# Optimization experiments

Hardware: AMD Instinct MI355X
Metric: run time of the kernel (lower is better)

The kernel has to match this reference:

```python
import jax, jax.numpy as jnp
import numpy as np

N, E, DIN, DH, DOUT, G = 100000, 1600000, 128, 128, 40, 512


def setup_inputs() -> dict:
    key = jax.random.key(0)
    ks = jax.random.split(key, 8)
    x = jax.random.normal(ks[0], (N, DIN), dtype=jnp.float32)
    src = jax.random.randint(ks[1], (E,), 0, N)
    dst = jax.random.randint(ks[2], (E,), 0, N)
    batch = jnp.sort(jax.random.randint(ks[3], (N,), 0, G))
    W1 = jax.random.normal(ks[4], (DIN, DH), dtype=jnp.float32) * (1.0 / np.sqrt(DIN))
    b1 = jnp.zeros((DH,), dtype=jnp.float32)
    W2 = jax.random.normal(ks[5], (DH, DOUT), dtype=jnp.float32) * (1.0 / np.sqrt(DH))
    b2 = jnp.zeros((DOUT,), dtype=jnp.float32)
    return {"x": x, "src": src, "dst": dst, "batch": batch,
            "W1": W1, "b1": b1, "W2": W2, "b2": b2, "num_graphs": G}


def gcn_conv(h, src, dst, n, W, b):
    # PyG GCNConv: linear transform, then D^-1/2 (A + I) D^-1/2 aggregation.
    h = h @ W  # [n, d_out]
    # degree on destination nodes, including self-loop weight 1
    deg = jax.ops.segment_sum(jnp.ones_like(dst, dtype=h.dtype), dst, num_segments=n) + 1.0
    dinv = jax.lax.rsqrt(deg)  # deg >= 1 so always finite
    coef = dinv[src] * dinv[dst]  # [E]
    agg = jax.ops.segment_sum(h[src] * coef[:, None], dst, num_segments=n)
    agg = agg + h * (dinv * dinv)[:, None]  # self-loop term
    return agg + b


def reference(x, src, dst, batch, W1, b1, W2, b2, num_graphs):
    n = x.shape[0]
    h = jax.nn.relu(gcn_conv(x, src, dst, n, W1, b1))  # dropout = identity (eval mode)
    h = jax.nn.relu(gcn_conv(h, src, dst, n, W2, b2))
    # global mean pool over graphs in the batch
    cnt = jax.ops.segment_sum(jnp.ones((n,), dtype=h.dtype), batch, num_segments=num_graphs)
    pooled = jax.ops.segment_sum(h, batch, num_segments=num_graphs) / jnp.maximum(cnt, 1.0)[:, None]
    return jax.nn.log_softmax(pooled, axis=1)
```

## Files before the change

### kernel.cpp

```cpp
#include <hip/hip_runtime.h>
#include <math.h>


typedef __attribute__((ext_vector_type(4))) float f32x4;
typedef __attribute__((ext_vector_type(2))) float f32x2;
typedef __attribute__((ext_vector_type(8))) short bf16x8;
typedef __attribute__((ext_vector_type(4))) uint uint4v;
typedef __attribute__((ext_vector_type(2))) uint uint2v;

constexpr int PAD = 64;
constexpr int CAP = 1536;
constexpr int NBMAX = 1600;

static __device__ __forceinline__ ushort f2bf(float f) {
    union { float f; uint u; } v{f};
    uint r = (v.u + 0x7FFF + ((v.u >> 16) & 1)) >> 16;
    return (ushort)r;
}
static __device__ __forceinline__ float bflo(uint v) {
    union { uint u; float f; } o{v << 16};
    return o.f;
}
static __device__ __forceinline__ float bfhi(uint v) {
    union { uint u; float f; } o{v & 0xffff0000u};
    return o.f;
}
static __device__ __forceinline__ uint packbf(float lo, float hi) {
    return ((uint)f2bf(hi) << 16) | (uint)f2bf(lo);
}

__global__ __launch_bounds__(1024) void k_binhist(
    const int* __restrict__ src, const int* __restrict__ dst, int E, int nbkt,
    int* __restrict__ cur2, int* __restrict__ bins,
    const float* __restrict__ W1, const float* __restrict__ W2,
    ushort* __restrict__ w1t, ushort* __restrict__ w2t, int histB) {
    __shared__ int lc[NBMAX];
    const int bid = blockIdx.x;
    const int t = threadIdx.x;
    if (bid >= histB) {
        int i = (bid - histB) * 1024 + t;
        if (i < 128 * 128) {
            int n = i >> 7, k = i & 127;
            w1t[i] = f2bf(W1[k * 128 + n]);
        } else if (i < 128 * 128 + 64 * 128) {
            int j = i - 128 * 128;
            int n = j >> 7, k = j & 127;
            w2t[j] = (n < 40) ? f2bf(W2[k * 40 + n]) : (ushort)0;
        }
        return;
    }
    for (int b = t; b < nbkt; b += 1024) lc[b] = 0;
    __syncthreads();
    const int elo = (int)(((long long)E * bid) / histB);
    const int ehi = (int)(((long long)E * (bid + 1)) / histB);
    for (int e = elo + t; e < ehi; e += 1024) {
        int d = __builtin_nontemporal_load(&dst[e]);
        atomicAdd(&lc[d >> 6], 1);
    }
    __syncthreads();
    for (int b = t; b < nbkt; b += 1024) {
        int c = lc[b];
        lc[b] = (c > 0) ? atomicAdd(&cur2[b], c) : 0;
    }
    __syncthreads();
    for (int e = elo + t; e < ehi; e += 1024) {
        int d = __builtin_nontemporal_load(&dst[e]);
        int s = __builtin_nontemporal_load(&src[e]);
        int b = d >> 6;
        int pos = atomicAdd(&lc[b], 1);
        if (pos < CAP) bins[(size_t)b * CAP + pos] = ((d & 63) << 17) | s;
    }
}

__global__ __launch_bounds__(256) void k_fillb(const int* __restrict__ cur2,
                                               const int* __restrict__ bins,
                                               int* __restrict__ degi,
                                               int* __restrict__ colidx, int N) {
    __shared__ int lcnt[64];
    const int b = blockIdx.x;
    const int base = b << 6;
    const int t = threadIdx.x;
    if (t < 64) lcnt[t] = 0;
    __syncthreads();
    int cnt = min(cur2[b], CAP);
    for (int i = t; i < cnt; i += 256) {
        int entry = bins[(size_t)b * CAP + i];
        int d = entry >> 17;
        int s = entry & 0x1FFFF;
        int r = atomicAdd(&lcnt[d], 1);
        if (r < PAD) colidx[((base + d) << 6) + r] = s;
    }
    __syncthreads();
    if (t < 64 && base + t < N) degi[base + t] = lcnt[t];
}

__global__ __launch_bounds__(256) void k_gemm1(const float* __restrict__ A,
                                               const ushort* __restrict__ BT,
                                               const int* __restrict__ degi,
                                               uint* __restrict__ g1u, int M) {
    __shared__ ushort As[64][136];
    __shared__ ushort Bs[128][136];
    const int tid = threadIdx.x;
    const int m0 = blockIdx.x * 64;
#pragma unroll
    for (int i = 0; i < 4; i++) {
        int chunk = tid + i * 256;
        int r = chunk >> 4, c8 = chunk & 15;
        float4 v0 = {0.f, 0.f, 0.f, 0.f}, v1 = {0.f, 0.f, 0.f, 0.f};
        if (m0 + r < M) {
            const float* p = &A[(size_t)(m0 + r) * 128 + c8 * 8];
            v0 = *(const float4*)p;
            v1 = *(const float4*)(p + 4);
        }
        ushort o[8];
        o[0] = f2bf(v0.x); o[1] = f2bf(v0.y); o[2] = f2bf(v0.z); o[3] = f2bf(v0.w);
        o[4] = f2bf(v1.x); o[5] = f2bf(v1.y); o[6] = f2bf(v1.z); o[7] = f2bf(v1.w);
        *(float4*)&As[r][c8 * 8] = *(float4*)o;
    }
#pragma unroll
    for (int i = 0; i < 8; i++) {
        int chunk = tid + i * 256;
        int r = chunk >> 4, c = chunk & 15;
        *(float4*)&Bs[r][c * 8] = *(const float4*)&BT[(size_t)r * 128 + c * 8];
    }
    __syncthreads();
    const int wave = tid >> 6, lane = tid & 63;
    const int arow = wave * 16 + (lane & 15);
    const int kgrp = (lane >> 4) * 8;
    f32x4 acc[8];
#pragma unroll
    for (int i = 0; i < 8; i++) acc[i] = (f32x4){0.f, 0.f, 0.f, 0.f};
#pragma unroll
    for (int kk = 0; kk < 4; kk++) {
        bf16x8 a = *(const bf16x8*)&As[arow][kk * 32 + kgrp];
#pragma unroll
        for (int nf = 0; nf < 8; nf++) {
            bf16x8 b = *(const bf16x8*)&Bs[nf * 16 + (lane & 15)][kk * 32 + kgrp];
            acc[nf] = __builtin_amdgcn_mfma_f32_16x16x32_bf16(b, a, acc[nf], 0, 0, 0);
        }
    }
    const int m = m0 + wave * 16 + (lane & 15);
    float dv = (m < M) ? rsqrtf((float)degi[m] + 1.0f) : 0.f;
#pragma unroll
    for (int nf = 0; nf < 8; nf++) {
        uint u = __builtin_amdgcn_cvt_pk_fp8_f32(dv * acc[nf][0], dv * acc[nf][1],
                                                 0, false);
        u = (uint)__builtin_amdgcn_cvt_pk_fp8_f32(dv * acc[nf][2], dv * acc[nf][3],
                                                  (int)u, true);
        if (m < M) g1u[(size_t)m * 32 + nf * 4 + (lane >> 4)] = u;
    }
}

__global__ __launch_bounds__(256) void k_agg128(const uint* __restrict__ g1u,
                                                const int* __restrict__ degi,
                                                const int* __restrict__ colidx,
                                                const float* __restrict__ bias,
                                                ushort* __restrict__ hout, int N) {
    __shared__ int sidx[4][64];
    const int w = threadIdx.x >> 6;
    const int lane = threadIdx.x & 63;
    const int wid = (blockIdx.x * 256 + threadIdx.x) >> 6;
    if (wid >= N) return;
    const int q = lane >> 4;
    const int l16 = lane & 15;
    const uint2v* hu = (const uint2v*)g1u;
    const int dg = degi[wid];
    const int cnt = min(dg, PAD);
    const int beg = wid << 6;
    float a0 = 0.f, a1 = 0.f, a2 = 0.f, a3 = 0.f;
    float a4 = 0.f, a5 = 0.f, a6 = 0.f, a7 = 0.f;
    if (lane < cnt) sidx[w][lane] = colidx[beg + lane];
    int i = 0;
    for (; i + 16 <= cnt; i += 16) {
        uint2v v[4];
#pragma unroll
        for (int k = 0; k < 4; k++) {
            v[k] = hu[(size_t)sidx[w][i + 4 * k + q] * 16 + l16];
        }
#pragma unroll
        for (int k = 0; k < 4; k++) {
            f32x2 d0 = __builtin_amdgcn_cvt_pk_f32_fp8(v[k].x, false);
            f32x2 d1 = __builtin_amdgcn_cvt_pk_f32_fp8(v[k].x, true);
            f32x2 d2 = __builtin_amdgcn_cvt_pk_f32_fp8(v[k].y, false);
            f32x2 d3 = __builtin_amdgcn_cvt_pk_f32_fp8(v[k].y, true);
            a0 += d0.x; a1 += d0.y; a2 += d1.x; a3 += d1.y;
            a4 += d2.x; a5 += d2.y; a6 += d3.x; a7 += d3.y;
        }
    }
    for (; i + q < cnt; i += 4) {
        uint2v vv = hu[(size_t)sidx[w][i + q] * 16 + l16];
        f32x2 d0 = __builtin_amdgcn_cvt_pk_f32_fp8(vv.x, false);
        f32x2 d1 = __builtin_amdgcn_cvt_pk_f32_fp8(vv.x, true);
        f32x2 d2 = __builtin_amdgcn_cvt_pk_f32_fp8(vv.y, false);
        f32x2 d3 = __builtin_amdgcn_cvt_pk_f32_fp8(vv.y, true);
        a0 += d0.x; a1 += d0.y; a2 += d1.x; a3 += d1.y;
        a4 += d2.x; a5 += d2.y; a6 += d3.x; a7 += d3.y;
    }
    a0 += __shfl_xor(a0, 16); a1 += __shfl_xor(a1, 16);
    a2 += __shfl_xor(a2, 16); a3 += __shfl_xor(a3, 16);
    a4 += __shfl_xor(a4, 16); a5 += __shfl_xor(a5, 16);
    a6 += __shfl_xor(a6, 16); a7 += __shfl_xor(a7, 16);
    a0 += __shfl_xor(a0, 32); a1 += __shfl_xor(a1, 32);
    a2 += __shfl_xor(a2, 32); a3 += __shfl_xor(a3, 32);
    a4 += __shfl_xor(a4, 32); a5 += __shfl_xor(a5, 32);
    a6 += __shfl_xor(a6, 32); a7 += __shfl_xor(a7, 32);
    if (lane < 16) {
        float dn = rsqrtf((float)dg + 1.0f);
        uint2v sv = hu[(size_t)wid * 16 + l16];
        {
            f32x2 d0 = __builtin_amdgcn_cvt_pk_f32_fp8(sv.x, false);
            f32x2 d1 = __builtin_amdgcn_cvt_pk_f32_fp8(sv.x, true);
            f32x2 d2 = __builtin_amdgcn_cvt_pk_f32_fp8(sv.y, false);
            f32x2 d3 = __builtin_amdgcn_cvt_pk_f32_fp8(sv.y, true);
            a0 += d0.x; a1 += d0.y; a2 += d1.x; a3 += d1.y;
            a4 += d2.x; a5 += d2.y; a6 += d3.x; a7 += d3.y;
        }
        float4 b0 = *(const float4*)&bias[l16 * 8];
        float4 b1v = *(const float4*)&bias[l16 * 8 + 4];
        a0 = dn * fmaxf(dn * a0 + b0.x, 0.f);
        a1 = dn * fmaxf(dn * a1 + b0.y, 0.f);
        a2 = dn * fmaxf(dn * a2 + b0.z, 0.f);
        a3 = dn * fmaxf(dn * a3 + b0.w, 0.f);
        a4 = dn * fmaxf(dn * a4 + b1v.x, 0.f);
        a5 = dn * fmaxf(dn * a5 + b1v.y, 0.f);
        a6 = dn * fmaxf(dn * a6 + b1v.z, 0.f);
        a7 = dn * fmaxf(dn * a7 + b1v.w, 0.f);
        uint4v o;
        o.x = packbf(a0, a1);
        o.y = packbf(a2, a3);
        o.z = packbf(a4, a5);
        o.w = packbf(a6, a7);
        __builtin_nontemporal_store(o, &((uint4v*)hout)[(size_t)wid * 16 + l16]);
    }
}

__global__ __launch_bounds__(256) void k_gemm_p(const ushort* __restrict__ A,
                                                const ushort* __restrict__ BT,
                                                uint* __restrict__ pu, int M) {
    __shared__ ushort As[64][136];
    __shared__ ushort Bs[64][136];
    const int tid = threadIdx.x;
    const int m0 = blockIdx.x * 64;
#pragma unroll
    for (int i = 0; i < 4; i++) {
        int chunk = tid + i * 256;
        int r = chunk >> 4, c = chunk & 15;
        float4 v = {0.f, 0.f, 0.f, 0.f};
        if (m0 + r < M) v = *(const float4*)&A[((size_t)(m0 + r)) * 128 + c * 8];
        *(float4*)&As[r][c * 8] = v;
    }
#pragma unroll
    for (int i = 0; i < 4; i++) {
        int chunk = tid + i * 256;
        int r = chunk >> 4, c = chunk & 15;
        *(float4*)&Bs[r][c * 8] = *(const float4*)&BT[(size_t)r * 128 + c * 8];
    }
    __syncthreads();
    const int wave = tid >> 6, lane = tid & 63;
    const int arow = wave * 16 + (lane & 15);
    const int kgrp = (lane >> 4) * 8;
    f32x4 acc[4];
#pragma unroll
    for (int i = 0; i < 4; i++) acc[i] = (f32x4){0.f, 0.f, 0.f, 0.f};
#pragma unroll
    for (int kk = 0; kk < 4; kk++) {
        bf16x8 a = *(const bf16x8*)&As[arow][kk * 32 + kgrp];
#pragma unroll
        for (int nf = 0; nf < 4; nf++) {
            bf16x8 b = *(const bf16x8*)&Bs[nf * 16 + (lane & 15)][kk * 32 + kgrp];
            acc[nf] = __builtin_amdgcn_mfma_f32_16x16x32_bf16(b, a, acc[nf], 0, 0, 0);
        }
    }
    const int m = m0 + wave * 16 + (lane & 15);
#pragma unroll
    for (int nf = 0; nf < 4; nf++) {
        uint u = __builtin_amdgcn_cvt_pk_fp8_f32(acc[nf][0], acc[nf][1], 0, false);
        u = (uint)__builtin_amdgcn_cvt_pk_fp8_f32(acc[nf][2], acc[nf][3], (int)u, true);
        if (m < M) pu[(size_t)m * 16 + nf * 4 + (lane >> 4)] = u;
    }
}

__global__ __launch_bounds__(256) void k_agg40(const uint* __restrict__ pu,
                                               const int* __restrict__ degi,
                                               const int* __restrict__ colidx,
                                               const float* __restrict__ b2,
                                               float* __restrict__ h2a, int N) {
    __shared__ int sidx[4][64];
    const int w = threadIdx.x >> 6;
    const int lane = threadIdx.x & 63;
    const int wid = (blockIdx.x * 256 + threadIdx.x) >> 6;
    if (wid >= N) return;
    const int q = lane >> 4;
    const int l16 = lane & 15;
    const int dg = degi[wid];
    const int cnt = min(dg, PAD);
    const int beg = wid << 6;
    float a0 = 0.f, a1 = 0.f, a2 = 0.f, a3 = 0.f;
    if (lane < cnt) sidx[w][lane] = colidx[beg + lane];
    int i = 0;
    for (; i + 16 <= cnt; i += 16) {
        uint v[4];
#pragma unroll
        for (int k = 0; k < 4; k++) {
            v[k] = pu[(size_t)sidx[w][i + 4 * k + q] * 16 + l16];
        }
#pragma unroll
        for (int k = 0; k < 4; k++) {
            f32x2 d0 = __builtin_amdgcn_cvt_pk_f32_fp8(v[k], false);
            f32x2 d1 = __builtin_amdgcn_cvt_pk_f32_fp8(v[k], true);
            a0 += d0.x; a1 += d0.y; a2 += d1.x; a3 += d1.y;
        }
    }
    for (; i + q < cnt; i += 4) {
        uint vv = pu[(size_t)sidx[w][i + q] * 16 + l16];
        f32x2 d0 = __builtin_amdgcn_cvt_pk_f32_fp8(vv, false);
        f32x2 d1 = __builtin_amdgcn_cvt_pk_f32_fp8(vv, true);
        a0 += d0.x; a1 += d0.y; a2 += d1.x; a3 += d1.y;
    }
    a0 += __shfl_xor(a0, 16); a1 += __shfl_xor(a1, 16);
    a2 += __shfl_xor(a2, 16); a3 += __shfl_xor(a3, 16);
    a0 += __shfl_xor(a0, 32); a1 += __shfl_xor(a1, 32);
    a2 += __shfl_xor(a2, 32); a3 += __shfl_xor(a3, 32);
    if (lane < 16 && l16 < 10) {
        float dn = rsqrtf((float)dg + 1.0f);
        uint sv = pu[(size_t)wid * 16 + l16];
        f32x2 d0 = __builtin_amdgcn_cvt_pk_f32_fp8(sv, false);
        f32x2 d1 = __builtin_amdgcn_cvt_pk_f32_fp8(sv, true);
        a0 += d0.x; a1 += d0.y; a2 += d1.x; a3 += d1.y;
        float4 bb = *(const float4*)&b2[l16 * 4];
        float4 o;
        o.x = fmaxf(dn * a0 + bb.x, 0.f);
        o.y = fmaxf(dn * a1 + bb.y, 0.f);
        o.z = fmaxf(dn * a2 + bb.z, 0.f);
        o.w = fmaxf(dn * a3 + bb.w, 0.f);
        *(float4*)&h2a[(size_t)wid * 40 + l16 * 4] = o;
    }
}

__global__ __launch_bounds__(256) void k_pool(const float* __restrict__ h2a,
                                              const int* __restrict__ batch, int N,
                                              int DOUT, float* __restrict__ out) {
    int g = blockIdx.x;
    int t = threadIdx.x;
    int lo = 0, hi = N;
    while (lo < hi) {
        int mid = (lo + hi) >> 1;
        if (batch[mid] < g) lo = mid + 1; else hi = mid;
    }
    int start = lo;
    hi = N;
    while (lo < hi) {
        int mid = (lo + hi) >> 1;
        if (batch[mid] <= g) lo = mid + 1; else hi = mid;
    }
    int end = lo;
    int cnt = end - start;
    int c = t & 63, rr = t >> 6;
    float acc = 0.f;
    if (c < DOUT) {
        for (int i = start + rr; i < end; i += 4) acc += h2a[(size_t)i * DOUT + c];
    }
    __shared__ float sm[4][64];
    sm[rr][c] = acc;
    __syncthreads();
    if (t < 64) {
        float v = (c < DOUT)
                      ? (sm[0][c] + sm[1][c] + sm[2][c] + sm[3][c]) / fmaxf((float)cnt, 1.f)
                      : -1e30f;
        float m = v;
#pragma unroll
        for (int o = 32; o; o >>= 1) m = fmaxf(m, __shfl_xor(m, o));
        float ex = (c < DOUT) ? expf(v - m) : 0.f;
        float s = ex;
#pragma unroll
        for (int o = 32; o; o >>= 1) s += __shfl_xor(s, o);
        if (c < DOUT) out[g * DOUT + c] = (v - m) - logf(s);
    }
}

extern "C" void kernel_launch(void* const* d_in, const int* in_sizes, int n_in,
                              void* d_out, int out_size, void* d_ws, size_t ws_size,
                              hipStream_t stream) {
    const float* x = (const float*)d_in[0];
    const int* src = (const int*)d_in[1];
    const int* dst = (const int*)d_in[2];
    const int* batch = (const int*)d_in[3];
    const float* W1 = (const float*)d_in[4];
    const float* b1 = (const float*)d_in[5];
    const float* W2 = (const float*)d_in[6];
    const float* b2 = (const float*)d_in[7];
    float* out = (float*)d_out;

    const int N = in_sizes[3];
    const int E = in_sizes[1];
    const int DOUT = in_sizes[7];
    const int G = out_size / DOUT;
    const int nbkt = (N + 63) >> 6;

    char* ws = (char*)d_ws;
    size_t off = 0;
    auto alloc = [&](size_t bytes) -> char* {
        char* p = ws + off;
        off += (bytes + 255) & ~(size_t)255;
        return p;
    };
    uint* g1u = (uint*)alloc((size_t)N * 128);
    ushort* g2 = (ushort*)alloc((size_t)N * 128 * 2);
    int* colidx = (int*)alloc((size_t)N * PAD * 4);
    int* bins = (int*)alloc((size_t)nbkt * CAP * 4);
    ushort* w1t = (ushort*)alloc(128 * 128 * 2);
    ushort* w2t = (ushort*)alloc(64 * 128 * 2);
    int* degi = (int*)alloc((size_t)N * 4);
    float* h2a = (float*)alloc((size_t)N * 40 * 4);
    char* z0 = ws + off;
    int* cur2 = (int*)alloc((size_t)nbkt * 4);
    size_t zlen = (size_t)((ws + off) - z0);

    uint* pu = g1u;

    hipMemsetAsync(z0, 0, zlen, stream);

    const int TB = 256;
    const int histB = 256;
    const int prepB = (128 * 128 + 64 * 128 + 1023) / 1024;
    k_binhist<<<histB + prepB, 1024, 0, stream>>>(src, dst, E, nbkt, cur2, bins,
                                                  W1, W2, w1t, w2t, histB);
    k_fillb<<<nbkt, TB, 0, stream>>>(cur2, bins, degi, colidx, N);
    k_gemm1<<<(N + 63) / 64, TB, 0, stream>>>(x, w1t, degi, g1u, N);
    k_agg128<<<(N + 3) / 4, TB, 0, stream>>>(g1u, degi, colidx, b1, g2, N);
    k_gemm_p<<<(N + 63) / 64, TB, 0, stream>>>(g2, w2t, pu, N);
    k_agg40<<<(N + 3) / 4, TB, 0, stream>>>(pu, degi, colidx, b2, h2a, N);
    k_pool<<<G, TB, 0, stream>>>(h2a, batch, N, DOUT, out);
}
```

Baseline: 191.7 us.

## Fuse layer-1 aggregation with layer-2 GEMM into a single kernel

Merges the 128-wide neighbor aggregation kernel with the following bf16 MFMA projection. Each block aggregates 16 nodes into a shared-memory tile and multiplies it by W2 there, so the bf16 intermediate no longer makes a round trip through global memory and one launch disappears. The fp8 accumulation is also rewritten to add packed float2 vectors directly, which may let the compiler emit packed adds. In exchange, each block does 16 rows, each wave walks four nodes in sequence, and every block reloads W2 into LDS, which raises LDS use and may reduce occupancy and latency hiding for the gathers.

Measured after the change: 189.7 us. Within noise of the previous version (-1.0%).

```diff
diff --git a/kernel.cpp b/kernel.cpp
--- a/kernel.cpp
+++ b/kernel.cpp
@@ -16,14 +16,6 @@
     union { float f; uint u; } v{f};
     uint r = (v.u + 0x7FFF + ((v.u >> 16) & 1)) >> 16;
     return (ushort)r;
-}
-static __device__ __forceinline__ float bflo(uint v) {
-    union { uint u; float f; } o{v << 16};
-    return o.f;
-}
-static __device__ __forceinline__ float bfhi(uint v) {
-    union { uint u; float f; } o{v & 0xffff0000u};
-    return o.f;
 }
 static __device__ __forceinline__ uint packbf(float lo, float hi) {
     return ((uint)f2bf(hi) << 16) | (uint)f2bf(lo);
@@ -151,133 +143,111 @@
     }
 }
 
-__global__ __launch_bounds__(256) void k_agg128(const uint* __restrict__ g1u,
-                                                const int* __restrict__ degi,
-                                                const int* __restrict__ colidx,
-                                                const float* __restrict__ bias,
-                                                ushort* __restrict__ hout, int N) {
+__global__ __launch_bounds__(256) void k_agg1p(const uint* __restrict__ g1u,
+                                               const int* __restrict__ degi,
+                                               const int* __restrict__ colidx,
+                                               const float* __restrict__ bias,
+                                               const ushort* __restrict__ w2t,
+                                               uint* __restrict__ pu, int N) {
+    __shared__ ushort g2t[16][136];
+    __shared__ ushort Bs[64][136];
     __shared__ int sidx[4][64];
-    const int w = threadIdx.x >> 6;
-    const int lane = threadIdx.x & 63;
-    const int wid = (blockIdx.x * 256 + threadIdx.x) >> 6;
-    if (wid >= N) return;
+    const int tid = threadIdx.x;
+    const int w = tid >> 6;
+    const int lane = tid & 63;
     const int q = lane >> 4;
     const int l16 = lane & 15;
     const uint2v* hu = (const uint2v*)g1u;
-    const int dg = degi[wid];
-    const int cnt = min(dg, PAD);
-    const int beg = wid << 6;
-    float a0 = 0.f, a1 = 0.f, a2 = 0.f, a3 = 0.f;
-    float a4 = 0.f, a5 = 0.f, a6 = 0.f, a7 = 0.f;
-    if (lane < cnt) sidx[w][lane] = colidx[beg + lane];
-    int i = 0;
-    for (; i + 16 <= cnt; i += 16) {
-        uint2v v[4];
-#pragma unroll
-        for (int k = 0; k < 4; k++) {
-            v[k] = hu[(size_t)sidx[w][i + 4 * k + q] * 16 + l16];
-        }
-#pragma unroll
-        for (int k = 0; k < 4; k++) {
-            f32x2 d0 = __builtin_amdgcn_cvt_pk_f32_fp8(v[k].x, false);
-            f32x2 d1 = __builtin_amdgcn_cvt_pk_f32_fp8(v[k].x, true);
-            f32x2 d2 = __builtin_amdgcn_cvt_pk_f32_fp8(v[k].y, false);
-            f32x2 d3 = __builtin_amdgcn_cvt_pk_f32_fp8(v[k].y, true);
-            a0 += d0.x; a1 += d0.y; a2 += d1.x; a3 += d1.y;
-            a4 += d2.x; a5 += d2.y; a6 += d3.x; a7 += d3.y;
-        }
-    }
-    for (; i + q < cnt; i += 4) {
-        uint2v vv = hu[(size_t)sidx[w][i + q] * 16 + l16];
-        f32x2 d0 = __builtin_amdgcn_cvt_pk_f32_fp8(vv.x, false);
-        f32x2 d1 = __builtin_amdgcn_cvt_pk_f32_fp8(vv.x, true);
-        f32x2 d2 = __builtin_amdgcn_cvt_pk_f32_fp8(vv.y, false);
-        f32x2 d3 = __builtin_amdgcn_cvt_pk_f32_fp8(vv.y, true);
-        a0 += d0.x; a1 += d0.y; a2 += d1.x; a3 += d1.y;
-        a4 += d2.x; a5 += d2.y; a6 += d3.x; a7 += d3.y;
-    }
-    a0 += __shfl_xor(a0, 16); a1 += __shfl_xor(a1, 16);
-    a2 += __shfl_xor(a2, 16); a3 += __shfl_xor(a3, 16);
-    a4 += __shfl_xor(a4, 16); a5 += __shfl_xor(a5, 16);
-    a6 += __shfl_xor(a6, 16); a7 += __shfl_xor(a7, 16);
-    a0 += __shfl_xor(a0, 32); a1 += __shfl_xor(a1, 32);
-    a2 += __shfl_xor(a2, 32); a3 += __shfl_xor(a3, 32);
-    a4 += __shfl_xor(a4, 32); a5 += __shfl_xor(a5, 32);
-    a6 += __shfl_xor(a6, 32); a7 += __shfl_xor(a7, 32);
-    if (lane < 16) {
-        float dn = rsqrtf((float)dg + 1.0f);
-        uint2v sv = hu[(size_t)wid * 16 + l16];
-        {
-            f32x2 d0 = __builtin_amdgcn_cvt_pk_f32_fp8(sv.x, false);
-            f32x2 d1 = __builtin_amdgcn_cvt_pk_f32_fp8(sv.x, true);
-            f32x2 d2 = __builtin_amdgcn_cvt_pk_f32_fp8(sv.y, false);
-            f32x2 d3 = __builtin_amdgcn_cvt_pk_f32_fp8(sv.y, true);
-            a0 += d0.x; a1 += d0.y; a2 += d1.x; a3 += d1.y;
-            a4 += d2.x; a5 += d2.y; a6 += d3.x; a7 += d3.y;
-        }
-        float4 b0 = *(const float4*)&bias[l16 * 8];
-        float4 b1v = *(const float4*)&bias[l16 * 8 + 4];
-        a0 = dn * fmaxf(dn * a0 + b0.x, 0.f);
-        a1 = dn * fmaxf(dn * a1 + b0.y, 0.f);
-        a2 = dn * fmaxf(dn * a2 + b0.z, 0.f);
-        a3 = dn * fmaxf(dn * a3 + b0.w, 0.f);
-        a4 = dn * fmaxf(dn * a4 + b1v.x, 0.f);
-        a5 = dn * fmaxf(dn * a5 + b1v.y, 0.f);
-        a6 = dn * fmaxf(dn * a6 + b1v.z, 0.f);
-        a7 = dn * fmaxf(dn * a7 + b1v.w, 0.f);
-        uint4v o;
-        o.x = packbf(a0, a1);
-        o.y = packbf(a2, a3);
-        o.z = packbf(a4, a5);
-        o.w = packbf(a6, a7);
-        __builtin_nontemporal_store(o, &((uint4v*)hout)[(size_t)wid * 16 + l16]);
-    }
-}
-
-__global__ __launch_bounds__(256) void k_gemm_p(const ushort* __restrict__ A,
-                                                const ushort* __restrict__ BT,
-                                                uint* __restrict__ pu, int M) {
-    __shared__ ushort As[64][136];
-    __shared__ ushort Bs[64][136];
-    const int tid = threadIdx.x;
-    const int m0 = blockIdx.x * 64;
+    const int tile0 = blockIdx.x * 16;
 #pragma unroll
     for (int i = 0; i < 4; i++) {
         int chunk = tid + i * 256;
         int r = chunk >> 4, c = chunk & 15;
-        float4 v = {0.f, 0.f, 0.f, 0.f};
-        if (m0 + r < M) v = *(const float4*)&A[((size_t)(m0 + r)) * 128 + c * 8];
-        *(float4*)&As[r][c * 8] = v;
-    }
-#pragma unroll
-    for (int i = 0; i < 4; i++) {
-        int chunk = tid + i * 256;
-        int r = chunk >> 4, c = chunk & 15;
-        *(float4*)&Bs[r][c * 8] = *(const float4*)&BT[(size_t)r * 128 + c * 8];
-    }
-    __syncthreads();
-    const int wave = tid >> 6, lane = tid & 63;
-    const int arow = wave * 16 + (lane & 15);
+        *(float4*)&Bs[r][c * 8] = *(const float4*)&w2t[(size_t)r * 128 + c * 8];
+    }
+#pragma unroll
+    for (int sub = 0; sub < 4; sub++) {
+        const int r = w * 4 + sub;
+        const int wid = tile0 + r;
+        f32x2 a0 = {0.f, 0.f}, a1 = {0.f, 0.f}, a2 = {0.f, 0.f}, a3 = {0.f, 0.f};
+        int dg = 0;
+        if (wid < N) {
+            dg = degi[wid];
+            const int cnt = min(dg, PAD);
+            const int beg = wid << 6;
+            if (lane < cnt) sidx[w][lane] = colidx[beg + lane];
+            int i = 0;
+            for (; i + 16 <= cnt; i += 16) {
+                uint2v v[4];
+#pragma unroll
+                for (int k = 0; k < 4; k++) {
+                    v[k] = hu[(size_t)sidx[w][i + 4 * k + q] * 16 + l16];
+                }
+#pragma unroll
+                for (int k = 0; k < 4; k++) {
+                    a0 += __builtin_amdgcn_cvt_pk_f32_fp8(v[k].x, false);
+                    a1 += __builtin_amdgcn_cvt_pk_f32_fp8(v[k].x, true);
+                    a2 += __builtin_amdgcn_cvt_pk_f32_fp8(v[k].y, false);
+                    a3 += __builtin_amdgcn_cvt_pk_f32_fp8(v[k].y, true);
+                }
+            }
+            for (; i + q < cnt; i += 4) {
+                uint2v vv = hu[(size_t)sidx[w][i + q] * 16 + l16];
+                a0 += __builtin_amdgcn_cvt_pk_f32_fp8(vv.x, false);
+                a1 += __builtin_amdgcn_cvt_pk_f32_fp8(vv.x, true);
+                a2 += __builtin_amdgcn_cvt_pk_f32_fp8(vv.y, false);
+                a3 += __builtin_amdgcn_cvt_pk_f32_fp8(vv.y, true);
+            }
+        }
+        a0.x += __shfl_xor(a0.x, 16); a0.y += __shfl_xor(a0.y, 16);
+        a1.x += __shfl_xor(a1.x, 16); a1.y += __shfl_xor(a1.y, 16);
+        a2.x += __shfl_xor(a2.x, 16); a2.y += __shfl_xor(a2.y, 16);
+        a3.x += __shfl_xor(a3.x, 16); a3.y += __shfl_xor(a3.y, 16);
+        a0.x += __shfl_xor(a0.x, 32); a0.y += __shfl_xor(a0.y, 32);
+        a1.x += __shfl_xor(a1.x, 32); a1.y += __shfl_xor(a1.y, 32);
+        a2.x += __shfl_xor(a2.x, 32); a2.y += __shfl_xor(a2.y, 32);
+        a3.x += __shfl_xor(a3.x, 32); a3.y += __shfl_xor(a3.y, 32);
+        if (lane < 16) {
+            float dn = rsqrtf((float)dg + 1.0f);
+            if (wid < N) {
+                uint2v sv = hu[(size_t)wid * 16 + l16];
+                a0 += __builtin_amdgcn_cvt_pk_f32_fp8(sv.x, false);
+                a1 += __builtin_amdgcn_cvt_pk_f32_fp8(sv.x, true);
+                a2 += __builtin_amdgcn_cvt_pk_f32_fp8(sv.y, false);
+                a3 += __builtin_amdgcn_cvt_pk_f32_fp8(sv.y, true);
+            }
+            float4 b0 = *(const float4*)&bias[l16 * 8];
+            float4 b1v = *(const float4*)&bias[l16 * 8 + 4];
+            float r0 = dn * fmaxf(dn * a0.x + b0.x, 0.f);
+            float r1 = dn * fmaxf(dn * a0.y + b0.y, 0.f);
+            float r2 = dn * fmaxf(dn * a1.x + b0.z, 0.f);
+            float r3 = dn * fmaxf(dn * a1.y + b0.w, 0.f);
+            float r4 = dn * fmaxf(dn * a2.x + b1v.x, 0.f);
+            float r5 = dn * fmaxf(dn * a2.y + b1v.y, 0.f);
+            float r6 = dn * fmaxf(dn * a3.x + b1v.z, 0.f);
+            float r7 = dn * fmaxf(dn * a3.y + b1v.w, 0.f);
+            uint4v o;
+            o.x = packbf(r0, r1);
+            o.y = packbf(r2, r3);
+            o.z = packbf(r4, r5);
+            o.w = packbf(r6, r7);
+            *(uint4v*)&g2t[r][l16 * 8] = o;
+        }
+    }
+    __syncthreads();
+    const int arow = lane & 15;
     const int kgrp = (lane >> 4) * 8;
-    f32x4 acc[4];
-#pragma unroll
-    for (int i = 0; i < 4; i++) acc[i] = (f32x4){0.f, 0.f, 0.f, 0.f};
+    f32x4 acc = {0.f, 0.f, 0.f, 0.f};
 #pragma unroll
     for (int kk = 0; kk < 4; kk++) {
-        bf16x8 a = *(const bf16x8*)&As[arow][kk * 32 + kgrp];
-#pragma unroll
-        for (int nf = 0; nf < 4; nf++) {
-            bf16x8 b = *(const bf16x8*)&Bs[nf * 16 + (lane & 15)][kk * 32 + kgrp];
-            acc[nf] = __builtin_amdgcn_mfma_f32_16x16x32_bf16(b, a, acc[nf], 0, 0, 0);
-        }
-    }
-    const int m = m0 + wave * 16 + (lane & 15);
-#pragma unroll
-    for (int nf = 0; nf < 4; nf++) {
-        uint u = __builtin_amdgcn_cvt_pk_fp8_f32(acc[nf][0], acc[nf][1], 0, false);
-        u = (uint)__builtin_amdgcn_cvt_pk_fp8_f32(acc[nf][2], acc[nf][3], (int)u, true);
-        if (m < M) pu[(size_t)m * 16 + nf * 4 + (lane >> 4)] = u;
-    }
+        bf16x8 a = *(const bf16x8*)&g2t[arow][kk * 32 + kgrp];
+        bf16x8 b = *(const bf16x8*)&Bs[w * 16 + (lane & 15)][kk * 32 + kgrp];
+        acc = __builtin_amdgcn_mfma_f32_16x16x32_bf16(b, a, acc, 0, 0, 0);
+    }
+    const int m = tile0 + (lane & 15);
+    uint u = __builtin_amdgcn_cvt_pk_fp8_f32(acc[0], acc[1], 0, false);
+    u = (uint)__builtin_amdgcn_cvt_pk_fp8_f32(acc[2], acc[3], (int)u, true);
+    if (m < N) pu[(size_t)m * 16 + w * 4 + (lane >> 4)] = u;
 }
 
 __global__ __launch_bounds__(256) void k_agg40(const uint* __restrict__ pu,
@@ -295,7 +265,7 @@
     const int dg = degi[wid];
     const int cnt = min(dg, PAD);
     const int beg = wid << 6;
-    float a0 = 0.f, a1 = 0.f, a2 = 0.f, a3 = 0.f;
+    f32x2 a01 = {0.f, 0.f}, a23 = {0.f, 0.f};
     if (lane < cnt) sidx[w][lane] = colidx[beg + lane];
     int i = 0;
     for (; i + 16 <= cnt; i += 16) {
@@ -306,33 +276,30 @@
         }
 #pragma unroll
         for (int k = 0; k < 4; k++) {
-            f32x2 d0 = __builtin_amdgcn_cvt_pk_f32_fp8(v[k], false);
-            f32x2 d1 = __builtin_amdgcn_cvt_pk_f32_fp8(v[k], true);
-            a0 += d0.x; a1 += d0.y; a2 += d1.x; a3 += d1.y;
+            a01 += __builtin_amdgcn_cvt_pk_f32_fp8(v[k], false);
+            a23 += __builtin_amdgcn_cvt_pk_f32_fp8(v[k], true);
         }
     }
     for (; i + q < cnt; i += 4) {
         uint vv = pu[(size_t)sidx[w][i + q] * 16 + l16];
-        f32x2 d0 = __builtin_amdgcn_cvt_pk_f32_fp8(vv, false);
-        f32x2 d1 = __builtin_amdgcn_cvt_pk_f32_fp8(vv, true);
-        a0 += d0.x; a1 += d0.y; a2 += d1.x; a3 += d1.y;
-    }
-    a0 += __shfl_xor(a0, 16); a1 += __shfl_xor(a1, 16);
-    a2 += __shfl_xor(a2, 16); a3 += __shfl_xor(a3, 16);
-    a0 += __shfl_xor(a0, 32); a1 += __shfl_xor(a1, 32);
-    a2 += __shfl_xor(a2, 32); a3 += __shfl_xor(a3, 32);
+        a01 += __builtin_amdgcn_cvt_pk_f32_fp8(vv, false);
+        a23 += __builtin_amdgcn_cvt_pk_f32_fp8(vv, true);
+    }
+    a01.x += __shfl_xor(a01.x, 16); a01.y += __shfl_xor(a01.y, 16);
+    a23.x += __shfl_xor(a23.x, 16); a23.y += __shfl_xor(a23.y, 16);
+    a01.x += __shfl_xor(a01.x, 32); a01.y += __shfl_xor(a01.y, 32);
+    a23.x += __shfl_xor(a23.x, 32); a23.y += __shfl_xor(a23.y, 32);
     if (lane < 16 && l16 < 10) {
         float dn = rsqrtf((float)dg + 1.0f);
         uint sv = pu[(size_t)wid * 16 + l16];
-        f32x2 d0 = __builtin_amdgcn_cvt_pk_f32_fp8(sv, false);
-        f32x2 d1 = __builtin_amdgcn_cvt_pk_f32_fp8(sv, true);
-        a0 += d0.x; a1 += d0.y; a2 += d1.x; a3 += d1.y;
+        a01 += __builtin_amdgcn_cvt_pk_f32_fp8(sv, false);
+        a23 += __builtin_amdgcn_cvt_pk_f32_fp8(sv, true);
         float4 bb = *(const float4*)&b2[l16 * 4];
         float4 o;
-        o.x = fmaxf(dn * a0 + bb.x, 0.f);
-        o.y = fmaxf(dn * a1 + bb.y, 0.f);
-        o.z = fmaxf(dn * a2 + bb.z, 0.f);
-        o.w = fmaxf(dn * a3 + bb.w, 0.f);
+        o.x = fmaxf(dn * a01.x + bb.x, 0.f);
+        o.y = fmaxf(dn * a01.y + bb.y, 0.f);
+        o.z = fmaxf(dn * a23.x + bb.z, 0.f);
+        o.w = fmaxf(dn * a23.y + bb.w, 0.f);
         *(float4*)&h2a[(size_t)wid * 40 + l16 * 4] = o;
     }
 }
@@ -405,7 +372,7 @@
         return p;
     };
     uint* g1u = (uint*)alloc((size_t)N * 128);
-    ushort* g2 = (ushort*)alloc((size_t)N * 128 * 2);
+    uint* pu = (uint*)alloc((size_t)N * 64);
     int* colidx = (int*)alloc((size_t)N * PAD * 4);
     int* bins = (int*)alloc((size_t)nbkt * CAP * 4);
     ushort* w1t = (ushort*)alloc(128 * 128 * 2);
@@ -416,8 +383,6 @@
     int* cur2 = (int*)alloc((size_t)nbkt * 4);
     size_t zlen = (size_t)((ws + off) - z0);
 
-    uint* pu = g1u;
-
     hipMemsetAsync(z0, 0, zlen, stream);
 
     const int TB = 256;
@@ -427,8 +392,7 @@
                                                   W1, W2, w1t, w2t, histB);
     k_fillb<<<nbkt, TB, 0, stream>>>(cur2, bins, degi, colidx, N);
     k_gemm1<<<(N + 63) / 64, TB, 0, stream>>>(x, w1t, degi, g1u, N);
-    k_agg128<<<(N + 3) / 4, TB, 0, stream>>>(g1u, degi, colidx, b1, g2, N);
-    k_gemm_p<<<(N + 63) / 64, TB, 0, stream>>>(g2, w2t, pu, N);
+    k_agg1p<<<(N + 15) / 16, TB, 0, stream>>>(g1u, degi, colidx, b1, w2t, pu, N);
     k_agg40<<<(N + 3) / 4, TB, 0, stream>>>(pu, degi, colidx, b2, h2a, N);
     k_pool<<<G, TB, 0, stream>>>(h2a, batch, N, DOUT, out);
 }
```
